# Kernel optimization log

Measured on AMD Instinct MI355X. Metric: run time of the kernel, lower is better.

The kernel has to match this reference:

```python
import jax, jax.numpy as jnp
import numpy as np

N = 100000   # nodes
E = 600000   # edges (no self loops by construction)
F = 64       # feature_size
H = 2 * F    # hidden_size = 128
G = 32       # graphs in batch
L = N // G   # nodes per graph (equal-size graphs)
NEG_SLOPE = 0.2  # GATConv default leaky_relu slope


def setup_inputs() -> dict:
    key = jax.random.key(0)
    ks = jax.random.split(key, 16)
    x = jax.random.normal(ks[0], (N, F), jnp.float32)
    # edges guaranteed to have no self loops (PyG GAT removes then re-adds them)
    src = jax.random.randint(ks[1], (E,), 0, N)
    off = jax.random.randint(ks[2], (E,), 1, N)
    dst = (src + off) % N
    edge_index = jnp.stack([src, dst]).astype(jnp.int32)
    batch = (jnp.arange(N) // L).astype(jnp.int32)
    sF = 1.0 / np.sqrt(F)
    sH = 1.0 / np.sqrt(H)
    return {
        "x": x, "edge_index": edge_index, "batch": batch,
        "W0": jax.random.normal(ks[3], (F, H), jnp.float32) * sF,
        "b0": jnp.zeros((H,), jnp.float32),
        "Wg": jax.random.normal(ks[4], (H, H), jnp.float32) * sH,
        "att_src": jax.random.normal(ks[5], (H,), jnp.float32) * sH,
        "att_dst": jax.random.normal(ks[6], (H,), jnp.float32) * sH,
        "W1": jax.random.normal(ks[7], (H, H), jnp.float32) * sH,
        "b1": jnp.zeros((H,), jnp.float32),
        "W2": jax.random.normal(ks[8], (H, H), jnp.float32) * sH,
        "b2": jnp.zeros((H,), jnp.float32),
        "Wr": jax.random.normal(ks[9], (H, F), jnp.float32) * sH,
        "br": jnp.zeros((F,), jnp.float32),
    }


def _gcn(x, row, col, w, W, b):
    # PyG GCNConv (normalize=True); edges already include self loops, w holds edge weights.
    xw = x @ W
    deg = jax.ops.segment_sum(w, col, num_segments=N)
    dinv = jnp.where(deg > 0, deg, 1.0) ** -0.5
    dinv = jnp.where(deg > 0, dinv, 0.0)
    norm = dinv[row] * w * dinv[col]                      # [E+N]
    out = jax.ops.segment_sum(xw[row] * norm[:, None], col, num_segments=N)
    return out + b


def reference(x, edge_index, batch, W0, b0, Wg, att_src, att_dst, W1, b1, W2, b2, Wr, br):
    row, col = edge_index[0], edge_index[1]
    loops = jnp.arange(N, dtype=edge_index.dtype)
    row_f = jnp.concatenate([row, loops])                 # [E+N] with self loops
    col_f = jnp.concatenate([col, loops])

    # initial GCNConv (gcn_norm adds self loops with weight 1) + relu
    x = jax.nn.relu(_gcn(x, row_f, col_f, jnp.ones(E + N, x.dtype), W0, b0))

    # GATConv attention (heads=1); node output is discarded in the torch module
    xg = x @ Wg
    a_s = xg @ att_src
    a_d = xg @ att_dst
    e = jax.nn.leaky_relu(a_s[row_f] + a_d[col_f], NEG_SLOPE)
    m = jax.ops.segment_max(e, col_f, num_segments=N)
    ex = jnp.exp(e - m[col_f])
    alpha = ex / jax.ops.segment_sum(ex, col_f, num_segments=N)[col_f]

    # gcn_norm's add_remaining_self_loops replaces self-loop weights with 1.0
    w = alpha.at[E:].set(1.0)

    x = jax.nn.relu(_gcn(x, row_f, col_f, w, W1, b1))
    x = jax.nn.relu(_gcn(x, row_f, col_f, w, W2, b2))

    # readout: Dropout (eval -> identity) + Linear
    out = x @ Wr + br                                     # [N, F]

    # unbatch + pad_sequence (batch_first=True); batch ids are sorted
    counts = jax.ops.segment_sum(jnp.ones(N, jnp.int32), batch, num_segments=G)
    starts = jnp.concatenate([jnp.zeros(1, jnp.int32), jnp.cumsum(counts)[:-1].astype(jnp.int32)])
    pos = jnp.arange(N, dtype=jnp.int32) - starts[batch]
    emb = jnp.zeros((G, L, F), out.dtype).at[batch, pos].set(out)
    return emb
```

## Files before the change

### kernel.cpp

```cpp
#include <hip/hip_runtime.h>
#include <hip/hip_bf16.h>
#include <math.h>

#define NN 100000
#define EE 600000
#define FF 64
#define HH 128
#define CHUNK 1024
#define NCHUNK ((NN + CHUNK - 1) / CHUNK)
#define NCHUNKS_M (NN / 16)

typedef unsigned short u16;
typedef __attribute__((ext_vector_type(8))) short bf16x8;
typedef __attribute__((ext_vector_type(4))) float f32x4;

__device__ __forceinline__ u16 f2bf(float f) {
    __hip_bfloat16 h = __float2bfloat16(f);
    return *(u16*)&h;
}
__device__ __forceinline__ float bf2f(u16 u) {
    unsigned int t = ((unsigned int)u) << 16;
    return *(float*)&t;
}


__global__ void count_k(const int* __restrict__ col, int* __restrict__ cnt) {
    int e = blockIdx.x * 256 + threadIdx.x;
    if (e < EE) atomicAdd(&cnt[col[e]], 1);
}

__global__ void chunksum_k(const int* __restrict__ cnt, int* __restrict__ chunk_sum,
                           float* __restrict__ dinv1) {
    int b = blockIdx.x, t = threadIdx.x;
    int base = b * CHUNK + t * 4;
    int s = 0;
    #pragma unroll
    for (int i = 0; i < 4; i++) {
        int idx = base + i;
        if (idx < NN) {
            int cv = cnt[idx];
            s += cv;
            dinv1[idx] = rsqrtf((float)cv + 1.0f);
        }
    }
    __shared__ int sm[4];
    for (int d = 32; d > 0; d >>= 1) s += __shfl_down(s, d);
    if ((t & 63) == 0) sm[t >> 6] = s;
    __syncthreads();
    if (t == 0) chunk_sum[b] = sm[0] + sm[1] + sm[2] + sm[3];
}

__global__ void chunkoff_k(const int* __restrict__ chunk_sum, int* __restrict__ chunk_off,
                           int* __restrict__ col_ptr) {
    if (threadIdx.x == 0) {
        int run = 0;
        for (int i = 0; i < NCHUNK; i++) { chunk_off[i] = run; run += chunk_sum[i]; }
        col_ptr[NN] = run;
    }
}

__global__ void colptr_k(const int* __restrict__ cnt, const int* __restrict__ chunk_off,
                         int* __restrict__ col_ptr, int* __restrict__ cursor) {
    int b = blockIdx.x, t = threadIdx.x;
    int base = b * CHUNK + t * 4;
    int c[4]; int tot = 0;
    #pragma unroll
    for (int i = 0; i < 4; i++) { int idx = base + i; c[i] = (idx < NN) ? cnt[idx] : 0; tot += c[i]; }
    __shared__ int s[256];
    s[t] = tot;
    __syncthreads();
    for (int d = 1; d < 256; d <<= 1) {
        int v = (t >= d) ? s[t - d] : 0;
        __syncthreads();
        s[t] += v;
        __syncthreads();
    }
    int excl = s[t] - tot;
    int off = chunk_off[b] + excl;
    int pre = 0;
    #pragma unroll
    for (int i = 0; i < 4; i++) {
        int idx = base + i;
        if (idx < NN) {
            col_ptr[idx] = off + pre;
            cursor[idx] = off + pre;
        }
        pre += c[i];
    }
}

__global__ void fill_k(const int* __restrict__ row, const int* __restrict__ col,
                       int* __restrict__ cursor, const float* __restrict__ dinv1,
                       int2* __restrict__ meta1) {
    int e = blockIdx.x * 256 + threadIdx.x;
    if (e < EE) {
        int r = row[e], c = col[e];
        int slot = atomicAdd(&cursor[c], 1);
        float w = dinv1[r] * dinv1[c];
        meta1[slot] = make_int2(r, __float_as_int(w));
    }
}


__global__ void prep_k(const float* __restrict__ W0, const float* __restrict__ W1,
                       const float* __restrict__ W2, const float* __restrict__ Wr,
                       const float* __restrict__ Wg, const float* __restrict__ att_src,
                       const float* __restrict__ att_dst, const float* __restrict__ x,
                       u16* __restrict__ Wt0, u16* __restrict__ Wt1,
                       u16* __restrict__ Wt2, u16* __restrict__ Wtr,
                       float* __restrict__ vs, float* __restrict__ vd,
                       u16* __restrict__ xb) {
    int i = blockIdx.x * 256 + threadIdx.x;
    if (i < NN * FF / 4) {
        float4 v = ((const float4*)x)[i];
        ushort4 o;
        o.x = f2bf(v.x); o.y = f2bf(v.y); o.z = f2bf(v.z); o.w = f2bf(v.w);
        ((ushort4*)xb)[i] = o;
        return;
    }
    i -= NN * FF / 4;
    if (i < 8192) {
        int n = i >> 6, k = i & 63;
        Wt0[i] = f2bf(W0[k * 128 + n]);
        return;
    }
    i -= 8192;
    if (i < 16384) {
        int n = i >> 7, k = i & 127;
        Wt1[i] = f2bf(W1[k * 128 + n]);
        return;
    }
    i -= 16384;
    if (i < 16384) {
        int n = i >> 7, k = i & 127;
        Wt2[i] = f2bf(W2[k * 128 + n]);
        return;
    }
    i -= 16384;
    if (i < 8192) {
        int n = i >> 7, k = i & 127;
        Wtr[i] = f2bf(Wr[k * 64 + n]);
        return;
    }
    i -= 8192;
    if (i < HH) {
        float s1 = 0.f, s2 = 0.f;
        for (int j = 0; j < HH; j++) {
            float w = Wg[i * HH + j];
            s1 += w * att_src[j];
            s2 += w * att_dst[j];
        }
        vs[i] = s1;
        vd[i] = s2;
    }
}


__global__ __launch_bounds__(256) void aggx_k(
    const u16* __restrict__ xb, const int* __restrict__ col_ptr, const int2* __restrict__ meta1,
    const float* __restrict__ dinv1, u16* __restrict__ xout) {
    int wid = threadIdx.x >> 6, lane = threadIdx.x & 63;
    int c = blockIdx.x * 4 + wid;
    if (c >= NN) return;
    int g = lane >> 3;
    int ch = (lane & 7) << 3;
    int beg = col_ptr[c], end = col_ptr[c + 1];
    float acc[8] = {};

    int p = beg + g;
    int r = 0; float w = 0.f;
    if (p < end) { int2 m = meta1[p]; r = m.x; w = __int_as_float(m.y); }
    while (p < end) {
        bf16x8 v = *(const bf16x8*)&xb[(size_t)r * FF + ch];
        int p2 = p + 8;
        int r2 = 0; float w2 = 0.f;
        if (p2 < end) { int2 m = meta1[p2]; r2 = m.x; w2 = __int_as_float(m.y); }
        #pragma unroll
        for (int j = 0; j < 8; j++) acc[j] = fmaf(bf2f((u16)v[j]), w, acc[j]);
        p = p2; r = r2; w = w2;
    }
    #pragma unroll
    for (int j = 0; j < 8; j++) {
        acc[j] += __shfl_xor(acc[j], 8);
        acc[j] += __shfl_xor(acc[j], 16);
        acc[j] += __shfl_xor(acc[j], 32);
    }

    if (g == 0) {
        bf16x8 v = *(const bf16x8*)&xb[(size_t)c * FF + ch];
        float dc = dinv1[c];
        float ws = dc * dc;
        bf16x8 o;
        #pragma unroll
        for (int j = 0; j < 8; j++) {
            float t = fmaf(bf2f((u16)v[j]), ws, acc[j]);
            o[j] = (short)f2bf(t);
        }
        *(bf16x8*)&xout[(size_t)c * FF + ch] = o;
    }
}


__global__ __launch_bounds__(256) void gemm1_k(const u16* __restrict__ A, const u16* __restrict__ Wt,
                                               const float* __restrict__ bias,
                                               const float* __restrict__ vs, const float* __restrict__ vd,
                                               u16* __restrict__ C, float* __restrict__ a_s,
                                               float* __restrict__ a_d) {
    constexpr int K = FF, N = HH, KK = K / 32, NT = N / 16;
    int lane = threadIdx.x & 63;
    int l15 = lane & 15, l4 = lane >> 4;
    int wg = blockIdx.x * 4 + (threadIdx.x >> 6);
    int nwaves = gridDim.x * 4;

    bf16x8 a_frag[KK][NT];
    #pragma unroll
    for (int kk = 0; kk < KK; kk++)
        #pragma unroll
        for (int nt = 0; nt < NT; nt++)
            a_frag[kk][nt] = *(const bf16x8*)&Wt[(size_t)(nt * 16 + l15) * K + kk * 32 + l4 * 8];
    f32x4 bias_f[NT], vs_f[NT], vd_f[NT];
    #pragma unroll
    for (int nt = 0; nt < NT; nt++) {
        bias_f[nt] = *(const f32x4*)&bias[nt * 16 + l4 * 4];
        vs_f[nt] = *(const f32x4*)&vs[nt * 16 + l4 * 4];
        vd_f[nt] = *(const f32x4*)&vd[nt * 16 + l4 * 4];
    }

    for (int ch = wg; ch < NCHUNKS_M; ch += nwaves) {
        int row = ch * 16 + l15;
        bf16x8 b_frag[KK];
        #pragma unroll
        for (int kk = 0; kk < KK; kk++)
            b_frag[kk] = *(const bf16x8*)&A[(size_t)row * K + kk * 32 + l4 * 8];
        f32x4 acc[NT] = {};
        #pragma unroll
        for (int kk = 0; kk < KK; kk++)
            #pragma unroll
            for (int nt = 0; nt < NT; nt++)
                acc[nt] = __builtin_amdgcn_mfma_f32_16x16x32_bf16(a_frag[kk][nt], b_frag[kk],
                                                                  acc[nt], 0, 0, 0);
        float s1 = 0.f, s2 = 0.f;
        #pragma unroll
        for (int nt = 0; nt < NT; nt++) {
            float o0 = fmaxf(acc[nt][0] + bias_f[nt][0], 0.f);
            float o1 = fmaxf(acc[nt][1] + bias_f[nt][1], 0.f);
            float o2 = fmaxf(acc[nt][2] + bias_f[nt][2], 0.f);
            float o3 = fmaxf(acc[nt][3] + bias_f[nt][3], 0.f);
            ushort4 o;
            o.x = f2bf(o0); o.y = f2bf(o1); o.z = f2bf(o2); o.w = f2bf(o3);
            *(ushort4*)&C[(size_t)row * N + nt * 16 + l4 * 4] = o;
            s1 += o0 * vs_f[nt][0] + o1 * vs_f[nt][1] + o2 * vs_f[nt][2] + o3 * vs_f[nt][3];
            s2 += o0 * vd_f[nt][0] + o1 * vd_f[nt][1] + o2 * vd_f[nt][2] + o3 * vd_f[nt][3];
        }
        s1 += __shfl_xor(s1, 16); s1 += __shfl_xor(s1, 32);
        s2 += __shfl_xor(s2, 16); s2 += __shfl_xor(s2, 32);
        if (l4 == 0) {
            a_s[row] = s1;
            a_d[row] = s2;
        }
    }
}


template <int K, int N, bool OUTF32>
__global__ __launch_bounds__(256) void mfma_gemm_k(const u16* __restrict__ A,
                                                   const u16* __restrict__ Wt,
                                                   const float* __restrict__ bias,
                                                   void* __restrict__ C_) {
    constexpr int KK = K / 32;
    constexpr int NT = N / 16;
    int lane = threadIdx.x & 63;
    int l15 = lane & 15, l4 = lane >> 4;
    int wg = blockIdx.x * 4 + (threadIdx.x >> 6);
    int nwaves = gridDim.x * 4;

    bf16x8 a_frag[KK][NT];
    #pragma unroll
    for (int kk = 0; kk < KK; kk++)
        #pragma unroll
        for (int nt = 0; nt < NT; nt++)
            a_frag[kk][nt] = *(const bf16x8*)&Wt[(size_t)(nt * 16 + l15) * K + kk * 32 + l4 * 8];

    f32x4 bias_f[NT];
    if (OUTF32) {
        #pragma unroll
        for (int nt = 0; nt < NT; nt++)
            bias_f[nt] = *(const f32x4*)&bias[nt * 16 + l4 * 4];
    }

    float* Cf = (float*)C_;
    u16* Cb = (u16*)C_;

    for (int ch = wg; ch < NCHUNKS_M; ch += nwaves) {
        int row = ch * 16 + l15;
        bf16x8 b_frag[KK];
        #pragma unroll
        for (int kk = 0; kk < KK; kk++)
            b_frag[kk] = *(const bf16x8*)&A[(size_t)row * K + kk * 32 + l4 * 8];
        f32x4 acc[NT] = {};
        #pragma unroll
        for (int kk = 0; kk < KK; kk++)
            #pragma unroll
            for (int nt = 0; nt < NT; nt++)
                acc[nt] = __builtin_amdgcn_mfma_f32_16x16x32_bf16(a_frag[kk][nt], b_frag[kk],
                                                                  acc[nt], 0, 0, 0);
        #pragma unroll
        for (int nt = 0; nt < NT; nt++) {
            int col = nt * 16 + l4 * 4;
            if (OUTF32) {
                float4 o;
                o.x = acc[nt][0] + bias_f[nt][0];
                o.y = acc[nt][1] + bias_f[nt][1];
                o.z = acc[nt][2] + bias_f[nt][2];
                o.w = acc[nt][3] + bias_f[nt][3];
                *(float4*)&Cf[(size_t)row * N + col] = o;
            } else {
                ushort4 o;
                o.x = f2bf(acc[nt][0]);
                o.y = f2bf(acc[nt][1]);
                o.z = f2bf(acc[nt][2]);
                o.w = f2bf(acc[nt][3]);
                *(ushort4*)&Cb[(size_t)row * N + col] = o;
            }
        }
    }
}


__global__ __launch_bounds__(256) void attn_k(const int* __restrict__ col_ptr,
                                              const int2* __restrict__ meta1,
                                              const float* __restrict__ a_s,
                                              const float* __restrict__ a_d,
                                              float* __restrict__ alpha,
                                              float* __restrict__ dinv2) {
    int lane = threadIdx.x & 63, wid = threadIdx.x >> 6;
    int grp = lane >> 3, idx = lane & 7;
    int c = blockIdx.x * 32 + wid * 8 + grp;
    if (c >= NN) return;
    int beg = col_ptr[c], end = col_ptr[c + 1];
    float ad = a_d[c];
    float es = a_s[c] + ad;
    es = (es > 0.f) ? es : 0.2f * es;
    float m = (idx == 0) ? es : -1e30f;
    float s = (idx == 0) ? 1.f : 0.f;
    for (int p = beg + idx; p < end; p += 8) {
        float e = a_s[meta1[p].x] + ad;
        e = (e > 0.f) ? e : 0.2f * e;
        alpha[p] = e;
        float mn = fmaxf(m, e);
        s = s * expf(m - mn) + expf(e - mn);
        m = mn;
    }
    #pragma unroll
    for (int d = 1; d < 8; d <<= 1) {
        float mo = __shfl_xor(m, d);
        float so = __shfl_xor(s, d);
        float mn = fmaxf(m, mo);
        s = s * expf(m - mn) + so * expf(mo - mn);
        m = mn;
    }
    float inv = 1.f / s;
    float aself = expf(es - m) * inv;
    float d2 = rsqrtf(2.f - aself);
    if (idx == 0) dinv2[c] = d2;
    float sc = inv * d2;
    for (int p = beg + idx; p < end; p += 8)
        alpha[p] = expf(alpha[p] - m) * sc;
}

__global__ void w2_k(const int2* __restrict__ meta1, const float* __restrict__ dinv2,
                     const float* __restrict__ alpha, int2* __restrict__ meta2) {
    int p = blockIdx.x * 256 + threadIdx.x;
    if (p < EE) {
        int r = meta1[p].x;
        float w = alpha[p] * dinv2[r];
        meta2[p] = make_int2(r, __float_as_int(w));
    }
}


__global__ __launch_bounds__(256) void agg2_k(
    const u16* __restrict__ xw, const int* __restrict__ col_ptr, const int2* __restrict__ meta2,
    const float* __restrict__ dinv2, const float* __restrict__ bias, u16* __restrict__ xout) {
    int wid = threadIdx.x >> 6, lane = threadIdx.x & 63;
    int c = blockIdx.x * 4 + wid;
    if (c >= NN) return;
    int g = lane >> 4;
    int ch = (lane & 15) << 3;
    int beg = col_ptr[c], end = col_ptr[c + 1];
    float acc[8] = {};

    int pA = beg + g, pB = pA + 4;
    int rA = 0, rB = 0; float wA = 0.f, wB = 0.f;
    if (pA < end) { int2 m = meta2[pA]; rA = m.x; wA = __int_as_float(m.y); }
    if (pB < end) { int2 m = meta2[pB]; rB = m.x; wB = __int_as_float(m.y); }
    while (pA < end) {
        bool hb = pB < end;
        bf16x8 vA = *(const bf16x8*)&xw[(size_t)rA * HH + ch];
        bf16x8 vB;
        if (hb) vB = *(const bf16x8*)&xw[(size_t)rB * HH + ch];
        int pA2 = pA + 8, pB2 = pB + 8;
        int rA2 = 0, rB2 = 0; float wA2 = 0.f, wB2 = 0.f;
        if (pA2 < end) { int2 m = meta2[pA2]; rA2 = m.x; wA2 = __int_as_float(m.y); }
        if (pB2 < end) { int2 m = meta2[pB2]; rB2 = m.x; wB2 = __int_as_float(m.y); }
        #pragma unroll
        for (int j = 0; j < 8; j++) acc[j] = fmaf(bf2f((u16)vA[j]), wA, acc[j]);
        if (hb) {
            #pragma unroll
            for (int j = 0; j < 8; j++) acc[j] = fmaf(bf2f((u16)vB[j]), wB, acc[j]);
        }
        pA = pA2; pB = pB2; rA = rA2; rB = rB2; wA = wA2; wB = wB2;
    }
    #pragma unroll
    for (int j = 0; j < 8; j++) {
        acc[j] += __shfl_xor(acc[j], 16);
        acc[j] += __shfl_xor(acc[j], 32);
    }

    if (g == 0) {
        bf16x8 v = *(const bf16x8*)&xw[(size_t)c * HH + ch];
        float dc = dinv2[c];
        float ws = dc * dc;
        f32x4 b4a = *(const f32x4*)&bias[ch];
        f32x4 b4b = *(const f32x4*)&bias[ch + 4];
        bf16x8 o;
        #pragma unroll
        for (int j = 0; j < 8; j++) {
            float bj = (j < 4) ? b4a[j] : b4b[j - 4];
            float t = fmaxf(fmaf(bf2f((u16)v[j]), ws, acc[j]) + bj, 0.f);
            o[j] = (short)f2bf(t);
        }
        *(bf16x8*)&xout[(size_t)c * HH + ch] = o;
    }
}


extern "C" void kernel_launch(void* const* d_in, const int* in_sizes, int n_in,
                              void* d_out, int out_size, void* d_ws, size_t ws_size,
                              hipStream_t stream) {
    const float* x = (const float*)d_in[0];
    const int* eidx = (const int*)d_in[1];
    const float* W0 = (const float*)d_in[3];
    const float* b0 = (const float*)d_in[4];
    const float* Wg = (const float*)d_in[5];
    const float* att_src = (const float*)d_in[6];
    const float* att_dst = (const float*)d_in[7];
    const float* W1 = (const float*)d_in[8];
    const float* b1 = (const float*)d_in[9];
    const float* W2 = (const float*)d_in[10];
    const float* b2 = (const float*)d_in[11];
    const float* Wr = (const float*)d_in[12];
    const float* br = (const float*)d_in[13];
    float* out = (float*)d_out;

    const int* erow = eidx;
    const int* ecol = eidx + EE;

    char* p = (char*)d_ws;
    auto alloc = [&](size_t bytes) {
        void* r = (void*)p;
        p += (bytes + 255) & ~(size_t)255;
        return r;
    };
    int* col_ptr = (int*)alloc((NN + 1) * sizeof(int));
    int2* meta1 = (int2*)alloc(EE * sizeof(int2));
    int2* meta2 = (int2*)alloc(EE * sizeof(int2));
    int* cnt = (int*)alloc(NN * sizeof(int));
    int* cursor = (int*)alloc(NN * sizeof(int));
    int* chunk_sum = (int*)alloc(128 * sizeof(int));
    int* chunk_off = (int*)alloc(128 * sizeof(int));
    float* alpha = (float*)alloc(EE * sizeof(float));
    float* dinv1 = (float*)alloc(NN * sizeof(float));
    float* dinv2 = (float*)alloc(NN * sizeof(float));
    float* a_s = (float*)alloc(NN * sizeof(float));
    float* a_d = (float*)alloc(NN * sizeof(float));
    float* vs = (float*)alloc(HH * sizeof(float));
    float* vd = (float*)alloc(HH * sizeof(float));
    u16* Wt0 = (u16*)alloc(8192 * sizeof(u16));
    u16* Wt1 = (u16*)alloc(16384 * sizeof(u16));
    u16* Wt2 = (u16*)alloc(16384 * sizeof(u16));
    u16* Wtr = (u16*)alloc(8192 * sizeof(u16));
    u16* xb = (u16*)alloc((size_t)NN * FF * sizeof(u16));
    u16* xaggb = (u16*)alloc((size_t)NN * FF * sizeof(u16));
    u16* bufA = (u16*)alloc((size_t)NN * HH * sizeof(u16));
    u16* bufB = (u16*)alloc((size_t)NN * HH * sizeof(u16));

    hipMemsetAsync(cnt, 0, NN * sizeof(int), stream);

    count_k<<<(EE + 255) / 256, 256, 0, stream>>>(ecol, cnt);
    chunksum_k<<<NCHUNK, 256, 0, stream>>>(cnt, chunk_sum, dinv1);
    chunkoff_k<<<1, 64, 0, stream>>>(chunk_sum, chunk_off, col_ptr);
    colptr_k<<<NCHUNK, 256, 0, stream>>>(cnt, chunk_off, col_ptr, cursor);
    fill_k<<<(EE + 255) / 256, 256, 0, stream>>>(erow, ecol, cursor, dinv1, meta1);
    prep_k<<<(NN * FF / 4 + 49280 + 255) / 256, 256, 0, stream>>>(
        W0, W1, W2, Wr, Wg, att_src, att_dst, x, Wt0, Wt1, Wt2, Wtr, vs, vd, xb);

    int aggGrid = (NN + 3) / 4;
    const int GG = 512;

    aggx_k<<<aggGrid, 256, 0, stream>>>(xb, col_ptr, meta1, dinv1, xaggb);
    gemm1_k<<<GG, 256, 0, stream>>>(xaggb, Wt0, b0, vs, vd, bufA, a_s, a_d);
    attn_k<<<(NN + 31) / 32, 256, 0, stream>>>(col_ptr, meta1, a_s, a_d, alpha, dinv2);
    w2_k<<<(EE + 255) / 256, 256, 0, stream>>>(meta1, dinv2, alpha, meta2);
    mfma_gemm_k<HH, HH, false><<<GG, 256, 0, stream>>>(bufA, Wt1, nullptr, bufB);
    agg2_k<<<aggGrid, 256, 0, stream>>>(bufB, col_ptr, meta2, dinv2, b1, bufA);
    mfma_gemm_k<HH, HH, false><<<GG, 256, 0, stream>>>(bufA, Wt2, nullptr, bufB);
    agg2_k<<<aggGrid, 256, 0, stream>>>(bufB, col_ptr, meta2, dinv2, b2, bufA);
    mfma_gemm_k<HH, FF, true><<<GG, 256, 0, stream>>>(bufA, Wtr, br, out);
}
```

Measured before the change: 277.8 us.

## Pack edge metadata into 32 bits, merge prep kernels, halve wave per node

Edge metadata shrinks from an int2 (row index plus fp32 weight) to one 32-bit word: the row index in the upper 17 bits and a truncated fp16 weight in the lower 15 bits, with the sign bit dropped because weights are non-negative. The degree-count kernel is merged with the weight and input conversion kernel to save a launch. Aggregation kernels now process two destination nodes per wave using half-waves, which cuts one shuffle-reduction step. This halves metadata traffic and improves lane use on low-degree nodes, at the cost of fp16 precision on edge weights.

```diff
diff --git a/kernel.cpp b/kernel.cpp
--- a/kernel.cpp
+++ b/kernel.cpp
@@ -1,5 +1,6 @@
 #include <hip/hip_runtime.h>
 #include <hip/hip_bf16.h>
+#include <hip/hip_fp16.h>
 #include <math.h>
 
 #define NN 100000
@@ -9,8 +10,10 @@
 #define CHUNK 1024
 #define NCHUNK ((NN + CHUNK - 1) / CHUNK)
 #define NCHUNKS_M (NN / 16)
+#define PREP_ITEMS (NN * FF / 4 + 49280)
 
 typedef unsigned short u16;
+typedef unsigned int u32;
 typedef __attribute__((ext_vector_type(8))) short bf16x8;
 typedef __attribute__((ext_vector_type(4))) float f32x4;
 
@@ -22,11 +25,73 @@
     unsigned int t = ((unsigned int)u) << 16;
     return *(float*)&t;
 }
-
-
-__global__ void count_k(const int* __restrict__ col, int* __restrict__ cnt) {
-    int e = blockIdx.x * 256 + threadIdx.x;
-    if (e < EE) atomicAdd(&cnt[col[e]], 1);
+__device__ __forceinline__ u32 enc_meta(int r, float w) {
+    u16 hb = __half_as_ushort(__float2half(w));
+    return ((u32)r << 15) | (hb & 0x7fffu);
+}
+__device__ __forceinline__ void dec_meta(u32 u, int& r, float& w) {
+    r = (int)(u >> 15);
+    w = __half2float(__ushort_as_half((u16)(u & 0x7fffu)));
+}
+
+
+__global__ void build_k(const int* __restrict__ col, int* __restrict__ cnt,
+                        const float* __restrict__ W0, const float* __restrict__ W1,
+                        const float* __restrict__ W2, const float* __restrict__ Wr,
+                        const float* __restrict__ Wg, const float* __restrict__ att_src,
+                        const float* __restrict__ att_dst, const float* __restrict__ x,
+                        u16* __restrict__ Wt0, u16* __restrict__ Wt1,
+                        u16* __restrict__ Wt2, u16* __restrict__ Wtr,
+                        float* __restrict__ vs, float* __restrict__ vd,
+                        u16* __restrict__ xb) {
+    int i = blockIdx.x * 256 + threadIdx.x;
+    if (i < EE) {
+        atomicAdd(&cnt[col[i]], 1);
+        return;
+    }
+    i -= EE;
+    if (i < NN * FF / 4) {
+        float4 v = ((const float4*)x)[i];
+        ushort4 o;
+        o.x = f2bf(v.x); o.y = f2bf(v.y); o.z = f2bf(v.z); o.w = f2bf(v.w);
+        ((ushort4*)xb)[i] = o;
+        return;
+    }
+    i -= NN * FF / 4;
+    if (i < 8192) {
+        int n = i >> 6, k = i & 63;
+        Wt0[i] = f2bf(W0[k * 128 + n]);
+        return;
+    }
+    i -= 8192;
+    if (i < 16384) {
+        int n = i >> 7, k = i & 127;
+        Wt1[i] = f2bf(W1[k * 128 + n]);
+        return;
+    }
+    i -= 16384;
+    if (i < 16384) {
+        int n = i >> 7, k = i & 127;
+        Wt2[i] = f2bf(W2[k * 128 + n]);
+        return;
+    }
+    i -= 16384;
+    if (i < 8192) {
+        int n = i >> 7, k = i & 127;
+        Wtr[i] = f2bf(Wr[k * 64 + n]);
+        return;
+    }
+    i -= 8192;
+    if (i < HH) {
+        float s1 = 0.f, s2 = 0.f;
+        for (int j = 0; j < HH; j++) {
+            float w = Wg[i * HH + j];
+            s1 += w * att_src[j];
+            s2 += w * att_dst[j];
+        }
+        vs[i] = s1;
+        vd[i] = s2;
+    }
 }
 
 __global__ void chunksum_k(const int* __restrict__ cnt, int* __restrict__ chunk_sum,
@@ -91,90 +156,36 @@
 
 __global__ void fill_k(const int* __restrict__ row, const int* __restrict__ col,
                        int* __restrict__ cursor, const float* __restrict__ dinv1,
-                       int2* __restrict__ meta1) {
+                       u32* __restrict__ meta1) {
     int e = blockIdx.x * 256 + threadIdx.x;
     if (e < EE) {
         int r = row[e], c = col[e];
         int slot = atomicAdd(&cursor[c], 1);
-        float w = dinv1[r] * dinv1[c];
-        meta1[slot] = make_int2(r, __float_as_int(w));
-    }
-}
-
-
-__global__ void prep_k(const float* __restrict__ W0, const float* __restrict__ W1,
-                       const float* __restrict__ W2, const float* __restrict__ Wr,
-                       const float* __restrict__ Wg, const float* __restrict__ att_src,
-                       const float* __restrict__ att_dst, const float* __restrict__ x,
-                       u16* __restrict__ Wt0, u16* __restrict__ Wt1,
-                       u16* __restrict__ Wt2, u16* __restrict__ Wtr,
-                       float* __restrict__ vs, float* __restrict__ vd,
-                       u16* __restrict__ xb) {
-    int i = blockIdx.x * 256 + threadIdx.x;
-    if (i < NN * FF / 4) {
-        float4 v = ((const float4*)x)[i];
-        ushort4 o;
-        o.x = f2bf(v.x); o.y = f2bf(v.y); o.z = f2bf(v.z); o.w = f2bf(v.w);
-        ((ushort4*)xb)[i] = o;
-        return;
-    }
-    i -= NN * FF / 4;
-    if (i < 8192) {
-        int n = i >> 6, k = i & 63;
-        Wt0[i] = f2bf(W0[k * 128 + n]);
-        return;
-    }
-    i -= 8192;
-    if (i < 16384) {
-        int n = i >> 7, k = i & 127;
-        Wt1[i] = f2bf(W1[k * 128 + n]);
-        return;
-    }
-    i -= 16384;
-    if (i < 16384) {
-        int n = i >> 7, k = i & 127;
-        Wt2[i] = f2bf(W2[k * 128 + n]);
-        return;
-    }
-    i -= 16384;
-    if (i < 8192) {
-        int n = i >> 7, k = i & 127;
-        Wtr[i] = f2bf(Wr[k * 64 + n]);
-        return;
-    }
-    i -= 8192;
-    if (i < HH) {
-        float s1 = 0.f, s2 = 0.f;
-        for (int j = 0; j < HH; j++) {
-            float w = Wg[i * HH + j];
-            s1 += w * att_src[j];
-            s2 += w * att_dst[j];
-        }
-        vs[i] = s1;
-        vd[i] = s2;
+        meta1[slot] = enc_meta(r, dinv1[r] * dinv1[c]);
     }
 }
 
 
 __global__ __launch_bounds__(256) void aggx_k(
-    const u16* __restrict__ xb, const int* __restrict__ col_ptr, const int2* __restrict__ meta1,
+    const u16* __restrict__ xb, const int* __restrict__ col_ptr, const u32* __restrict__ meta1,
     const float* __restrict__ dinv1, u16* __restrict__ xout) {
     int wid = threadIdx.x >> 6, lane = threadIdx.x & 63;
-    int c = blockIdx.x * 4 + wid;
-    if (c >= NN) return;
-    int g = lane >> 3;
-    int ch = (lane & 7) << 3;
+    int sub = lane >> 5;
+    int c = blockIdx.x * 8 + wid * 2 + sub;
+    int hl = lane & 31;
+    int g = hl >> 3;
+    int ch = (hl & 7) << 3;
     int beg = col_ptr[c], end = col_ptr[c + 1];
     float acc[8] = {};
 
     int p = beg + g;
     int r = 0; float w = 0.f;
-    if (p < end) { int2 m = meta1[p]; r = m.x; w = __int_as_float(m.y); }
+    if (p < end) dec_meta(meta1[p], r, w);
     while (p < end) {
         bf16x8 v = *(const bf16x8*)&xb[(size_t)r * FF + ch];
-        int p2 = p + 8;
+        int p2 = p + 4;
         int r2 = 0; float w2 = 0.f;
-        if (p2 < end) { int2 m = meta1[p2]; r2 = m.x; w2 = __int_as_float(m.y); }
+        if (p2 < end) dec_meta(meta1[p2], r2, w2);
         #pragma unroll
         for (int j = 0; j < 8; j++) acc[j] = fmaf(bf2f((u16)v[j]), w, acc[j]);
         p = p2; r = r2; w = w2;
@@ -183,7 +194,6 @@
     for (int j = 0; j < 8; j++) {
         acc[j] += __shfl_xor(acc[j], 8);
         acc[j] += __shfl_xor(acc[j], 16);
-        acc[j] += __shfl_xor(acc[j], 32);
     }
 
     if (g == 0) {
@@ -328,7 +338,7 @@
 
 
 __global__ __launch_bounds__(256) void attn_k(const int* __restrict__ col_ptr,
-                                              const int2* __restrict__ meta1,
+                                              const u32* __restrict__ meta1,
                                               const float* __restrict__ a_s,
                                               const float* __restrict__ a_d,
                                               float* __restrict__ alpha,
@@ -344,7 +354,7 @@
     float m = (idx == 0) ? es : -1e30f;
     float s = (idx == 0) ? 1.f : 0.f;
     for (int p = beg + idx; p < end; p += 8) {
-        float e = a_s[meta1[p].x] + ad;
+        float e = a_s[meta1[p] >> 15] + ad;
         e = (e > 0.f) ? e : 0.2f * e;
         alpha[p] = e;
         float mn = fmaxf(m, e);
@@ -368,41 +378,44 @@
         alpha[p] = expf(alpha[p] - m) * sc;
 }
 
-__global__ void w2_k(const int2* __restrict__ meta1, const float* __restrict__ dinv2,
-                     const float* __restrict__ alpha, int2* __restrict__ meta2) {
+__global__ void w2_k(const u32* __restrict__ meta1, const float* __restrict__ dinv2,
+                     const float* __restrict__ alpha, u32* __restrict__ meta2) {
     int p = blockIdx.x * 256 + threadIdx.x;
     if (p < EE) {
-        int r = meta1[p].x;
+        u32 u = meta1[p];
+        int r = (int)(u >> 15);
         float w = alpha[p] * dinv2[r];
-        meta2[p] = make_int2(r, __float_as_int(w));
+        u16 hb = __half_as_ushort(__float2half(w));
+        meta2[p] = (u & 0xffff8000u) | (hb & 0x7fffu);
     }
 }
 
 
 __global__ __launch_bounds__(256) void agg2_k(
-    const u16* __restrict__ xw, const int* __restrict__ col_ptr, const int2* __restrict__ meta2,
+    const u16* __restrict__ xw, const int* __restrict__ col_ptr, const u32* __restrict__ meta2,
     const float* __restrict__ dinv2, const float* __restrict__ bias, u16* __restrict__ xout) {
     int wid = threadIdx.x >> 6, lane = threadIdx.x & 63;
-    int c = blockIdx.x * 4 + wid;
-    if (c >= NN) return;
-    int g = lane >> 4;
-    int ch = (lane & 15) << 3;
+    int sub = lane >> 5;
+    int c = blockIdx.x * 8 + wid * 2 + sub;
+    int hl = lane & 31;
+    int g = hl >> 4;
+    int ch = (hl & 15) << 3;
     int beg = col_ptr[c], end = col_ptr[c + 1];
     float acc[8] = {};
 
-    int pA = beg + g, pB = pA + 4;
+    int pA = beg + g, pB = pA + 2;
     int rA = 0, rB = 0; float wA = 0.f, wB = 0.f;
-    if (pA < end) { int2 m = meta2[pA]; rA = m.x; wA = __int_as_float(m.y); }
-    if (pB < end) { int2 m = meta2[pB]; rB = m.x; wB = __int_as_float(m.y); }
+    if (pA < end) dec_meta(meta2[pA], rA, wA);
+    if (pB < end) dec_meta(meta2[pB], rB, wB);
     while (pA < end) {
         bool hb = pB < end;
         bf16x8 vA = *(const bf16x8*)&xw[(size_t)rA * HH + ch];
         bf16x8 vB;
         if (hb) vB = *(const bf16x8*)&xw[(size_t)rB * HH + ch];
-        int pA2 = pA + 8, pB2 = pB + 8;
+        int pA2 = pA + 4, pB2 = pB + 4;
         int rA2 = 0, rB2 = 0; float wA2 = 0.f, wB2 = 0.f;
-        if (pA2 < end) { int2 m = meta2[pA2]; rA2 = m.x; wA2 = __int_as_float(m.y); }
-        if (pB2 < end) { int2 m = meta2[pB2]; rB2 = m.x; wB2 = __int_as_float(m.y); }
+        if (pA2 < end) dec_meta(meta2[pA2], rA2, wA2);
+        if (pB2 < end) dec_meta(meta2[pB2], rB2, wB2);
         #pragma unroll
         for (int j = 0; j < 8; j++) acc[j] = fmaf(bf2f((u16)vA[j]), wA, acc[j]);
         if (hb) {
@@ -412,10 +425,7 @@
         pA = pA2; pB = pB2; rA = rA2; rB = rB2; wA = wA2; wB = wB2;
     }
     #pragma unroll
-    for (int j = 0; j < 8; j++) {
-        acc[j] += __shfl_xor(acc[j], 16);
-        acc[j] += __shfl_xor(acc[j], 32);
-    }
+    for (int j = 0; j < 8; j++) acc[j] += __shfl_xor(acc[j], 16);
 
     if (g == 0) {
         bf16x8 v = *(const bf16x8*)&xw[(size_t)c * HH + ch];
@@ -463,8 +473,8 @@
         return r;
     };
     int* col_ptr = (int*)alloc((NN + 1) * sizeof(int));
-    int2* meta1 = (int2*)alloc(EE * sizeof(int2));
-    int2* meta2 = (int2*)alloc(EE * sizeof(int2));
+    u32* meta1 = (u32*)alloc(EE * sizeof(u32));
+    u32* meta2 = (u32*)alloc(EE * sizeof(u32));
     int* cnt = (int*)alloc(NN * sizeof(int));
     int* cursor = (int*)alloc(NN * sizeof(int));
     int* chunk_sum = (int*)alloc(128 * sizeof(int));
@@ -487,15 +497,15 @@
 
     hipMemsetAsync(cnt, 0, NN * sizeof(int), stream);
 
-    count_k<<<(EE + 255) / 256, 256, 0, stream>>>(ecol, cnt);
+    build_k<<<(EE + PREP_ITEMS + 255) / 256, 256, 0, stream>>>(
+        ecol, cnt, W0, W1, W2, Wr, Wg, att_src, att_dst, x,
+        Wt0, Wt1, Wt2, Wtr, vs, vd, xb);
     chunksum_k<<<NCHUNK, 256, 0, stream>>>(cnt, chunk_sum, dinv1);
     chunkoff_k<<<1, 64, 0, stream>>>(chunk_sum, chunk_off, col_ptr);
     colptr_k<<<NCHUNK, 256, 0, stream>>>(cnt, chunk_off, col_ptr, cursor);
     fill_k<<<(EE + 255) / 256, 256, 0, stream>>>(erow, ecol, cursor, dinv1, meta1);
-    prep_k<<<(NN * FF / 4 + 49280 + 255) / 256, 256, 0, stream>>>(
-        W0, W1, W2, Wr, Wg, att_src, att_dst, x, Wt0, Wt1, Wt2, Wtr, vs, vd, xb);
-
-    int aggGrid = (NN + 3) / 4;
+
+    int aggGrid = NN / 8;
     const int GG = 512;
 
     aggx_k<<<aggGrid, 256, 0, stream>>>(xb, col_ptr, meta1, dinv1, xaggb);
```

Result: faster. 247.8 us (-10.8%).
